# Performance work log

Hardware: AMD Instinct MI355X
Metric: run time of the kernel (lower is better)

## Reference

```python
import jax, jax.numpy as jnp
import numpy as np

E, H = 1024, 16
B, N = 4, 2048
D = E // H

def setup_inputs() -> dict:
    key = jax.random.key(0)
    ks = jax.random.split(key, 5)
    s = 1.0 / np.sqrt(E)
    return {
        "x": jax.random.normal(ks[0], (B, N, E), dtype=jnp.float32),
        "Wqkv": jax.random.normal(ks[1], (E, 3 * E), dtype=jnp.float32) * s,
        "bqkv": jnp.zeros((3 * E,), dtype=jnp.float32),
        "Wproj": jax.random.normal(ks[2], (E, E), dtype=jnp.float32) * s,
        "bproj": jnp.zeros((E,), dtype=jnp.float32),
    }

def reference(x, Wqkv, bqkv, Wproj, bproj):
    b, n, e = x.shape
    qkv = x @ Wqkv + bqkv  # [b, n, 3e]
    # torch rearrange 'b n (h d qkv) -> qkv b h n d': last dim splits as (h, d, 3)
    qkv = qkv.reshape(b, n, H, D, 3)
    qkv = jnp.transpose(qkv, (4, 0, 2, 1, 3))  # [3, b, h, n, d]
    q, k, v = qkv[0], qkv[1], qkv[2]
    # NOTE: module scales by 1/sqrt(e) (full embed dim), faithfully reproduced
    att = jax.nn.softmax(jnp.einsum('bhqd,bhkd->bhqk', q, k) / jnp.sqrt(jnp.float32(E)), axis=-1)
    out = jnp.einsum('bhqk,bhkd->bhqd', att, v)  # dropout is identity in eval
    out = jnp.transpose(out, (0, 2, 1, 3)).reshape(b, n, e)  # 'b h n d -> b n (h d)'
    return out @ Wproj + bproj
```

## Files before the change

### kernel.cpp

```cpp
#include <hip/hip_runtime.h>
#include <stdint.h>

typedef unsigned short u16;
typedef __attribute__((ext_vector_type(8))) short short8;
typedef __attribute__((ext_vector_type(4))) float f32x4;

#define LOG2E 1.44269504088896340736f
#define CS (0.03125f * LOG2E)
#define BB 4
#define NN 2048
#define EE 1024
#define HH 16
#define DD 64
#define MM 8192
#define C3 3072

#if __has_builtin(__builtin_amdgcn_exp2f)
#define EXP2(x) __builtin_amdgcn_exp2f(x)
#else
#define EXP2(x) exp2f(x)
#endif

__device__ __forceinline__ u16 f2bf(float f) {
  union { float f; unsigned u; } v; v.f = f;
  unsigned r = v.u + 0x7fffu + ((v.u >> 16) & 1u);
  return (u16)(r >> 16);
}

#if __has_builtin(__builtin_amdgcn_cvt_pk_bf16_f32)
typedef __attribute__((ext_vector_type(2))) __bf16 bf16x2;
__device__ __forceinline__ unsigned pk2(float a, float b) {
  union { bf16x2 v; unsigned u; } c;
  c.v = __builtin_amdgcn_cvt_pk_bf16_f32(a, b);
  return c.u;
}
#else
__device__ __forceinline__ unsigned pk2(float a, float b) {
  union { float f; unsigned u; } x, y; x.f = a; y.f = b;
  return ((x.u + 0x8000u) >> 16) | ((y.u + 0x8000u) & 0xffff0000u);
}
#endif

__device__ __forceinline__ void async16(const void* g, void* l) {
  __builtin_amdgcn_global_load_lds((const __attribute__((address_space(1))) void*)g,
                                   (__attribute__((address_space(3))) void*)l,
                                   16, 0, 0);
}

__device__ __forceinline__ int vperm(int t) {
  return (t & 0x23) | ((t & 8) << 1) | ((t & 4) << 1) | ((t & 16) >> 2);
}

__global__ __launch_bounds__(256) void prep_kernel(const float* __restrict__ x, u16* __restrict__ xb,
                                                   const float* __restrict__ Wqkv, u16* __restrict__ WqkvT,
                                                   const float* __restrict__ Wproj, u16* __restrict__ WprojT) {
  __shared__ float tile[32][33];
  const int bid = blockIdx.x;
  if (bid < 8192) {
    int i = (bid * 256 + threadIdx.x) * 4;
    float4 v = *(const float4*)(x + i);
    ushort4 o; o.x = f2bf(v.x); o.y = f2bf(v.y); o.z = f2bf(v.z); o.w = f2bf(v.w);
    *(ushort4*)(xb + i) = o;
    return;
  }
  const int permute = bid < 11264 ? 1 : 0;
  const float* W = permute ? Wqkv : Wproj;
  u16* Wt = permute ? WqkvT : WprojT;
  const int ncols = permute ? C3 : EE;
  const int t = permute ? bid - 8192 : bid - 11264;
  const int nbx = permute ? 96 : 32;
  const int c0 = (t % nbx) * 32, k0 = (t / nbx) * 32;
  const int tx = threadIdx.x & 31, ty = threadIdx.x >> 5;
#pragma unroll
  for (int r = 0; r < 32; r += 8)
    tile[ty + r][tx] = W[(size_t)(k0 + ty + r) * ncols + c0 + tx];
  __syncthreads();
#pragma unroll
  for (int r = 0; r < 32; r += 8) {
    int c = c0 + ty + r;
    int cp = c;
    if (permute) {
      int tt = c % 3, hh = c / 192, d = (c / 3) % 64;
      cp = tt * 1024 + hh * 64 + d;
    }
    Wt[(size_t)cp * EE + k0 + tx] = f2bf(tile[tx][ty + r]);
  }
}

template <int KDIM, int MI>
__device__ __forceinline__ void gemm_core(const u16* __restrict__ A, const u16* __restrict__ Bt,
                                          int m0, int n0, u16* As, u16* Bs, f32x4 (*acc)[4]) {
  constexpr int L2M = (MI == 8) ? 3 : 2;
  constexpr int ACH = MI * 128;
  constexpr int ALD = MI / 2;
  constexpr int ASZ = ACH * 8;
  constexpr int NT = KDIM / 32;
  const int tid = threadIdx.x, lane = tid & 63, wave = tid >> 6;
  const int wm = wave >> 1, wn = wave & 1;

#pragma unroll
  for (int i = 0; i < MI; i++)
#pragma unroll
    for (int j = 0; j < 4; j++) acc[i][j] = (f32x4){0.f, 0.f, 0.f, 0.f};

  auto stage = [&](int t, int slot) {
    const u16* Ab = A + (size_t)m0 * KDIM + t * 32;
    const u16* Bb = Bt + (size_t)n0 * KDIM + t * 32;
#pragma unroll
    for (int i = 0; i < ALD; i++) {
      int c = i * 256 + tid;
      int r = c & 15, qc = (c >> 4) & 3, mi = (c >> 6) & (MI - 1), wmc = c >> (6 + L2M);
      int row = (wmc * MI + mi) * 16 + r;
      async16(Ab + (size_t)row * KDIM + qc * 8, &As[slot * ASZ + c * 8]);
    }
#pragma unroll
    for (int i = 0; i < 2; i++) {
      int c = i * 256 + tid;
      int r = c & 15, qc = (c >> 4) & 3, ci = (c >> 6) & 3, wnc = c >> 8;
      int row = (wnc * 4 + ci) * 16 + r;
      async16(Bb + (size_t)row * KDIM + qc * 8, &Bs[slot * 4096 + c * 8]);
    }
  };

  stage(0, 0);
  stage(1, 1);
  if constexpr (MI == 8) asm volatile("s_waitcnt vmcnt(6)" ::: "memory");
  else                   asm volatile("s_waitcnt vmcnt(4)" ::: "memory");
  __builtin_amdgcn_s_barrier();

  for (int t = 0; t < NT; ++t) {
    const int slot = t % 3;
    if (t + 2 < NT) stage(t + 2, (t + 2) % 3);
    short8 af[MI], bf[4];
    const u16* Ar = As + slot * ASZ + (wm * (MI * 64) + lane) * 8;
#pragma unroll
    for (int mi = 0; mi < MI; mi++) af[mi] = *(const short8*)(Ar + mi * 512);
    const u16* Br = Bs + slot * 4096 + (wn * 256 + lane) * 8;
#pragma unroll
    for (int ci = 0; ci < 4; ci++) bf[ci] = *(const short8*)(Br + ci * 512);
    __builtin_amdgcn_s_setprio(1);
#pragma unroll
    for (int mi = 0; mi < MI; mi++)
#pragma unroll
      for (int ci = 0; ci < 4; ci++)
        acc[mi][ci] = __builtin_amdgcn_mfma_f32_16x16x32_bf16(af[mi], bf[ci], acc[mi][ci], 0, 0, 0);
    __builtin_amdgcn_s_setprio(0);
    if (t + 2 < NT) {
      if constexpr (MI == 8) asm volatile("s_waitcnt vmcnt(6)" ::: "memory");
      else                   asm volatile("s_waitcnt vmcnt(4)" ::: "memory");
      __builtin_amdgcn_s_barrier();
    } else if (t + 1 < NT) {
      asm volatile("s_waitcnt vmcnt(0)" ::: "memory");
      __builtin_amdgcn_s_barrier();
    }
  }
}


__global__ __launch_bounds__(256, 2) void gemm_qkv(const u16* __restrict__ Xb, const u16* __restrict__ Wt,
                                                   const float* __restrict__ bqkv, u16* __restrict__ Qb,
                                                   u16* __restrict__ KVt) {
  __shared__ __align__(16) u16 As[3 * 8192];
  __shared__ __align__(16) u16 Bs[3 * 4096];
  f32x4 acc[8][4];
  const int m0 = blockIdx.y * 256, n0 = blockIdx.x * 128;
  gemm_core<EE, 8>(Xb, Wt, m0, n0, As, Bs, acc);
  const int tid = threadIdx.x, lane = tid & 63, wave = tid >> 6;
  const int q = lane >> 4, r16 = lane & 15;
  const int wm = wave >> 1, wn = wave & 1;
  const int wrow = wm * 128, wcol = wn * 64;
  const int t = n0 >> 10;
  const int b = m0 >> 11;
#pragma unroll
  for (int ci = 0; ci < 4; ci++) {
    const int cp = n0 + wcol + ci * 16 + r16;
    const int hh = (cp >> 6) & 15, d = cp & 63;
    const float bias = bqkv[hh * 192 + d * 3 + t];
    if (t == 0) {
#pragma unroll
      for (int mi = 0; mi < 8; mi++)
#pragma unroll
        for (int r = 0; r < 4; r++) {
          const int m = m0 + wrow + mi * 16 + q * 4 + r;
          Qb[((size_t)(b * 16 + hh) * 2048 + (m & 2047)) * 64 + d] = f2bf((acc[mi][ci][r] + bias) * CS);
        }
    } else if (t == 1) {
      const size_t bhbase = (size_t)(b * 16 + hh) * 32;
      const size_t dpart = (size_t)(d >> 5) * 2048 + ((d >> 3) & 3) * 128 + (d & 7);
#pragma unroll
      for (int mi = 0; mi < 8; mi++)
#pragma unroll
        for (int r = 0; r < 4; r++) {
          const int key = (m0 + wrow + mi * 16 + q * 4 + r) & 2047;
          KVt[(bhbase + (key >> 6)) * 8192 + dpart + ((key >> 4) & 3) * 512 + (key & 15) * 8] =
              f2bf(acc[mi][ci][r] + bias);
        }
    } else {
      const size_t bhbase = (size_t)(b * 16 + hh) * 32;
      const int dpart = (d >> 4) * 512 + (d & 15) * 8;
#pragma unroll
      for (int mi = 0; mi < 8; mi++) {
        const int nb = (m0 + wrow + mi * 16 + q * 4) & 2047;
        const int sb = vperm(nb & 63);
        ushort4 w;
        w.x = f2bf(acc[mi][ci][0] + bias);
        w.y = f2bf(acc[mi][ci][1] + bias);
        w.z = f2bf(acc[mi][ci][2] + bias);
        w.w = f2bf(acc[mi][ci][3] + bias);
        *(ushort4*)&KVt[(bhbase + (nb >> 6)) * 8192 + 4096 + (sb >> 5) * 2048 +
                        ((sb >> 3) & 3) * 128 + dpart + (sb & 7)] = w;
      }
    }
  }
}

__global__ __launch_bounds__(256, 3) void gemm_proj(const u16* __restrict__ Ob, const u16* __restrict__ Wt,
                                                    const float* __restrict__ bp, float* __restrict__ out) {
  __shared__ __align__(16) u16 As[3 * 4096];
  __shared__ __align__(16) u16 Bs[3 * 4096];
  f32x4 acc[4][4];
  const int m0 = blockIdx.y * 128, n0 = blockIdx.x * 128;
  gemm_core<EE, 4>(Ob, Wt, m0, n0, As, Bs, acc);
  const int tid = threadIdx.x, lane = tid & 63, wave = tid >> 6;
  const int q = lane >> 4, r16 = lane & 15;
  const int wrow = (wave >> 1) * 64, wcol = (wave & 1) * 64;
#pragma unroll
  for (int ci = 0; ci < 4; ci++) {
    const int col = n0 + wcol + ci * 16 + r16;
    const float bias = bp[col];
#pragma unroll
    for (int mi = 0; mi < 4; mi++)
#pragma unroll
      for (int r = 0; r < 4; r++) {
        const int m = m0 + wrow + mi * 16 + q * 4 + r;
        out[(size_t)m * EE + col] = acc[mi][ci][r] + bias;
      }
  }
}

__global__ __launch_bounds__(256, 4) void attn_kernel(const u16* __restrict__ Qg, const u16* __restrict__ KVg,
                                                      u16* __restrict__ Ob) {
  __shared__ __align__(16) u16 KVd[2][8192];
  const int tid = threadIdx.x, lane = tid & 63, wave = tid >> 6;
  const int q = lane >> 4, r16 = lane & 15;
  const int id = blockIdx.x + 16 * blockIdx.y;
  const int g = id & 7, s = id >> 3;
  const int bh = g * 8 + (s >> 4);
  const int q0 = (s & 15) * 128;
  const u16* Qp = Qg + ((size_t)bh * NN + q0) * DD;
  const u16* KVp = KVg + (size_t)bh * (32 * 8192);

  short8 qf[2][2];
#pragma unroll
  for (int nj = 0; nj < 2; nj++)
#pragma unroll
    for (int ks = 0; ks < 2; ks++)
      qf[nj][ks] = *(const short8*)(Qp + (wave * 32 + nj * 16 + r16) * 64 + ks * 32 + q * 8);

#pragma unroll
  for (int i = 0; i < 4; i++) {
    int c = i * 256 + tid;
    async16(KVp + c * 8, &KVd[0][c * 8]);
  }
  __syncthreads();

  f32x4 o[2][4];
  f32x4 ol[2];
#pragma unroll
  for (int i = 0; i < 2; i++) {
    ol[i] = (f32x4){0.f, 0.f, 0.f, 0.f};
#pragma unroll
    for (int j = 0; j < 4; j++) o[i][j] = (f32x4){0.f, 0.f, 0.f, 0.f};
  }
  const short8 ones = {16256, 16256, 16256, 16256, 16256, 16256, 16256, 16256};

  for (int j = 0; j < 32; j++) {
    const int buf = j & 1;
    if (j < 31) {
      const u16* src = KVp + (size_t)(j + 1) * 8192;
#pragma unroll
      for (int i = 0; i < 4; i++) {
        int c = i * 256 + tid;
        async16(src + c * 8, &KVd[buf ^ 1][c * 8]);
      }
    }

    f32x4 st[4][2];
#pragma unroll
    for (int mi = 0; mi < 4; mi++)
#pragma unroll
      for (int nj = 0; nj < 2; nj++) st[mi][nj] = (f32x4){0.f, 0.f, 0.f, 0.f};
#pragma unroll
    for (int ks = 0; ks < 2; ks++) {
      short8 kf[4];
#pragma unroll
      for (int mi = 0; mi < 4; mi++)
        kf[mi] = *(const short8*)&KVd[buf][ks * 2048 + mi * 512 + lane * 8];
#pragma unroll
      for (int mi = 0; mi < 4; mi++)
#pragma unroll
        for (int nj = 0; nj < 2; nj++)
          st[mi][nj] = __builtin_amdgcn_mfma_f32_16x16x32_bf16(kf[mi], qf[nj][ks], st[mi][nj], 0, 0, 0);
    }

    uint2 pka[4][2];
#pragma unroll
    for (int mi = 0; mi < 4; mi++)
#pragma unroll
      for (int nj = 0; nj < 2; nj++) {
        float p0 = EXP2(st[mi][nj][0]);
        float p1 = EXP2(st[mi][nj][1]);
        float p2 = EXP2(st[mi][nj][2]);
        float p3 = EXP2(st[mi][nj][3]);
        pka[mi][nj].x = pk2(p0, p1);
        pka[mi][nj].y = pk2(p2, p3);
      }

#pragma unroll
    for (int kp = 0; kp < 2; kp++) {
      short8 vf[4];
#pragma unroll
      for (int ci = 0; ci < 4; ci++)
        vf[ci] = *(const short8*)&KVd[buf][4096 + kp * 2048 + ci * 512 + lane * 8];
#pragma unroll
      for (int ri = 0; ri < 2; ri++) {
        union { uint4 u; short8 s; } a;
        a.u.x = pka[2 * kp][ri].x;
        a.u.y = pka[2 * kp][ri].y;
        a.u.z = pka[2 * kp + 1][ri].x;
        a.u.w = pka[2 * kp + 1][ri].y;
#pragma unroll
        for (int ci = 0; ci < 4; ci++)
          o[ri][ci] = __builtin_amdgcn_mfma_f32_16x16x32_bf16(a.s, vf[ci], o[ri][ci], 0, 0, 0);
        ol[ri] = __builtin_amdgcn_mfma_f32_16x16x32_bf16(a.s, ones, ol[ri], 0, 0, 0);
      }
    }

    __syncthreads();
  }

  const int b = bh >> 4, h = bh & 15;
#pragma unroll
  for (int ri = 0; ri < 2; ri++)
#pragma unroll
    for (int r = 0; r < 4; r++) {
      const float inv = 1.0f / ol[ri][r];
      const int n = q0 + wave * 32 + ri * 16 + q * 4 + r;
#pragma unroll
      for (int ci = 0; ci < 4; ci++) {
        const int d = ci * 16 + r16;
        Ob[((size_t)(b * NN + n)) * EE + h * 64 + d] = f2bf(o[ri][ci][r] * inv);
      }
    }
}


extern "C" void kernel_launch(void* const* d_in, const int* in_sizes, int n_in,
                              void* d_out, int out_size, void* d_ws, size_t ws_size,
                              hipStream_t stream) {
  const float* x     = (const float*)d_in[0];
  const float* Wqkv  = (const float*)d_in[1];
  const float* bqkv  = (const float*)d_in[2];
  const float* Wproj = (const float*)d_in[3];
  const float* bproj = (const float*)d_in[4];
  float* out = (float*)d_out;
  char* ws = (char*)d_ws;

  u16* Xb     = (u16*)(ws);
  u16* Ob     = Xb;
  u16* Qb     = (u16*)(ws + (size_t)(16 << 20));
  u16* KVt    = (u16*)(ws + (size_t)(32 << 20));
  u16* WqkvT  = (u16*)(ws + (size_t)(64 << 20));
  u16* WprojT = (u16*)(ws + (size_t)(72 << 20));

  prep_kernel<<<12288, 256, 0, stream>>>(x, Xb, Wqkv, WqkvT, Wproj, WprojT);
  gemm_qkv<<<dim3(24, 32), 256, 0, stream>>>(Xb, WqkvT, bqkv, Qb, KVt);
  attn_kernel<<<dim3(16, 64), 256, 0, stream>>>(Qb, KVt, Ob);
  gemm_proj<<<dim3(8, 64), 256, 0, stream>>>(Ob, WprojT, bproj, out);
}
```

Measured before the change: 299.2 us.

## Rework both GEMMs into 256x256 8-wave tiles with interleaved quarter-step prefetch

```diff
diff --git a/kernel.cpp b/kernel.cpp
--- a/kernel.cpp
+++ b/kernel.cpp
@@ -87,93 +87,157 @@
   }
 }
 
-template <int KDIM, int MI>
-__device__ __forceinline__ void gemm_core(const u16* __restrict__ A, const u16* __restrict__ Bt,
-                                          int m0, int n0, u16* As, u16* Bs, f32x4 (*acc)[4]) {
-  constexpr int L2M = (MI == 8) ? 3 : 2;
-  constexpr int ACH = MI * 128;
-  constexpr int ALD = MI / 2;
-  constexpr int ASZ = ACH * 8;
-  constexpr int NT = KDIM / 32;
+template <int KDIM>
+__device__ __forceinline__ void gemm_core8(const u16* __restrict__ A, const u16* __restrict__ Bt,
+                                           int m0, int n0, u16* As, u16* Bs, f32x4 (*acc)[4]) {
+  constexpr int NT = KDIM / 64;
   const int tid = threadIdx.x, lane = tid & 63, wave = tid >> 6;
-  const int wm = wave >> 1, wn = wave & 1;
-
-#pragma unroll
-  for (int i = 0; i < MI; i++)
+  const int wm = wave >> 2, wn = wave & 3;
+
+#pragma unroll
+  for (int i = 0; i < 8; i++)
 #pragma unroll
     for (int j = 0; j < 4; j++) acc[i][j] = (f32x4){0.f, 0.f, 0.f, 0.f};
 
-  auto stage = [&](int t, int slot) {
-    const u16* Ab = A + (size_t)m0 * KDIM + t * 32;
-    const u16* Bb = Bt + (size_t)n0 * KDIM + t * 32;
-#pragma unroll
-    for (int i = 0; i < ALD; i++) {
-      int c = i * 256 + tid;
-      int r = c & 15, qc = (c >> 4) & 3, mi = (c >> 6) & (MI - 1), wmc = c >> (6 + L2M);
-      int row = (wmc * MI + mi) * 16 + r;
-      async16(Ab + (size_t)row * KDIM + qc * 8, &As[slot * ASZ + c * 8]);
-    }
+  auto stageA = [&](int t, int h) {
+    const u16* Ab = A + (size_t)m0 * KDIM + t * 64;
+    u16* dst = As + (t & 1) * 16384;
 #pragma unroll
     for (int i = 0; i < 2; i++) {
-      int c = i * 256 + tid;
-      int r = c & 15, qc = (c >> 4) & 3, ci = (c >> 6) & 3, wnc = c >> 8;
-      int row = (wnc * 4 + ci) * 16 + r;
-      async16(Bb + (size_t)row * KDIM + qc * 8, &Bs[slot * 4096 + c * 8]);
+      int j = i * 512 + tid;
+      int lj = j & 63, mi_l = (j >> 6) & 3, wmj = (j >> 8) & 1, ksj = (j >> 9) & 1;
+      int mi = h * 4 + mi_l;
+      int c = ((ksj * 2 + wmj) * 8 + mi) * 64 + lj;
+      int row = wmj * 128 + mi * 16 + (lj & 15);
+      int k = ksj * 32 + (lj >> 4) * 8;
+      async16(Ab + (size_t)row * KDIM + k, dst + c * 8);
     }
   };
-
-  stage(0, 0);
-  stage(1, 1);
-  if constexpr (MI == 8) asm volatile("s_waitcnt vmcnt(6)" ::: "memory");
-  else                   asm volatile("s_waitcnt vmcnt(4)" ::: "memory");
+  auto stageB = [&](int t, int cset) {
+    const u16* Bb = Bt + (size_t)n0 * KDIM + t * 64;
+    u16* dst = Bs + (t & 1) * 16384;
+#pragma unroll
+    for (int i = 0; i < 2; i++) {
+      int j = i * 512 + tid;
+      int lj = j & 63, ci_l = (j >> 6) & 1, wnj = (j >> 7) & 3, ksj = (j >> 9) & 1;
+      int ci = cset * 2 + ci_l;
+      int c = ((ksj * 4 + wnj) * 4 + ci) * 64 + lj;
+      int row = wnj * 64 + ci * 16 + (lj & 15);
+      int k = ksj * 32 + (lj >> 4) * 8;
+      async16(Bb + (size_t)row * KDIM + k, dst + c * 8);
+    }
+  };
+
+  stageA(0, 0); stageB(0, 0); stageB(0, 1); stageA(0, 1);
+  asm volatile("s_waitcnt vmcnt(4)" ::: "memory");
   __builtin_amdgcn_s_barrier();
 
+  short8 af[4][2], bf[4][2];
+#pragma unroll 2
   for (int t = 0; t < NT; ++t) {
-    const int slot = t % 3;
-    if (t + 2 < NT) stage(t + 2, (t + 2) % 3);
-    short8 af[MI], bf[4];
-    const u16* Ar = As + slot * ASZ + (wm * (MI * 64) + lane) * 8;
-#pragma unroll
-    for (int mi = 0; mi < MI; mi++) af[mi] = *(const short8*)(Ar + mi * 512);
-    const u16* Br = Bs + slot * 4096 + (wn * 256 + lane) * 8;
-#pragma unroll
-    for (int ci = 0; ci < 4; ci++) bf[ci] = *(const short8*)(Br + ci * 512);
+    const int buf = t & 1;
+    const u16* Ab = As + buf * 16384;
+    const u16* Bb = Bs + buf * 16384;
+    const bool pf = (t + 1 < NT);
+
+#pragma unroll
+    for (int m = 0; m < 4; m++)
+#pragma unroll
+      for (int ks = 0; ks < 2; ks++)
+        af[m][ks] = *(const short8*)&Ab[(((ks * 2 + wm) * 8 + m) * 64 + lane) * 8];
+#pragma unroll
+    for (int c = 0; c < 2; c++)
+#pragma unroll
+      for (int ks = 0; ks < 2; ks++)
+        bf[c][ks] = *(const short8*)&Bb[(((ks * 4 + wn) * 4 + c) * 64 + lane) * 8];
+    if (pf) stageA(t + 1, 0);
+    __builtin_amdgcn_s_barrier();
     __builtin_amdgcn_s_setprio(1);
 #pragma unroll
-    for (int mi = 0; mi < MI; mi++)
-#pragma unroll
-      for (int ci = 0; ci < 4; ci++)
-        acc[mi][ci] = __builtin_amdgcn_mfma_f32_16x16x32_bf16(af[mi], bf[ci], acc[mi][ci], 0, 0, 0);
+    for (int m = 0; m < 4; m++)
+#pragma unroll
+      for (int c = 0; c < 2; c++)
+#pragma unroll
+        for (int ks = 0; ks < 2; ks++)
+          acc[m][c] = __builtin_amdgcn_mfma_f32_16x16x32_bf16(af[m][ks], bf[c][ks], acc[m][c], 0, 0, 0);
     __builtin_amdgcn_s_setprio(0);
-    if (t + 2 < NT) {
-      if constexpr (MI == 8) asm volatile("s_waitcnt vmcnt(6)" ::: "memory");
-      else                   asm volatile("s_waitcnt vmcnt(4)" ::: "memory");
+    if (pf) asm volatile("s_waitcnt vmcnt(4)" ::: "memory");
+    else    asm volatile("s_waitcnt vmcnt(2)" ::: "memory");
+    __builtin_amdgcn_s_barrier();
+
+#pragma unroll
+    for (int c = 2; c < 4; c++)
+#pragma unroll
+      for (int ks = 0; ks < 2; ks++)
+        bf[c][ks] = *(const short8*)&Bb[(((ks * 4 + wn) * 4 + c) * 64 + lane) * 8];
+    if (pf) stageB(t + 1, 0);
+    __builtin_amdgcn_s_barrier();
+    __builtin_amdgcn_s_setprio(1);
+#pragma unroll
+    for (int m = 0; m < 4; m++)
+#pragma unroll
+      for (int c = 2; c < 4; c++)
+#pragma unroll
+        for (int ks = 0; ks < 2; ks++)
+          acc[m][c] = __builtin_amdgcn_mfma_f32_16x16x32_bf16(af[m][ks], bf[c][ks], acc[m][c], 0, 0, 0);
+    __builtin_amdgcn_s_setprio(0);
+    if (pf) asm volatile("s_waitcnt vmcnt(4)" ::: "memory");
+    else    asm volatile("s_waitcnt vmcnt(0)" ::: "memory");
+    __builtin_amdgcn_s_barrier();
+
+#pragma unroll
+    for (int m = 0; m < 4; m++)
+#pragma unroll
+      for (int ks = 0; ks < 2; ks++)
+        af[m][ks] = *(const short8*)&Ab[(((ks * 2 + wm) * 8 + 4 + m) * 64 + lane) * 8];
+    if (pf) stageB(t + 1, 1);
+    __builtin_amdgcn_s_barrier();
+    __builtin_amdgcn_s_setprio(1);
+#pragma unroll
+    for (int m = 0; m < 4; m++)
+#pragma unroll
+      for (int c = 0; c < 2; c++)
+#pragma unroll
+        for (int ks = 0; ks < 2; ks++)
+          acc[4 + m][c] = __builtin_amdgcn_mfma_f32_16x16x32_bf16(af[m][ks], bf[c][ks], acc[4 + m][c], 0, 0, 0);
+    __builtin_amdgcn_s_setprio(0);
+    __builtin_amdgcn_s_barrier();
+
+    if (pf) stageA(t + 1, 1);
+    __builtin_amdgcn_s_barrier();
+    __builtin_amdgcn_s_setprio(1);
+#pragma unroll
+    for (int m = 0; m < 4; m++)
+#pragma unroll
+      for (int c = 2; c < 4; c++)
+#pragma unroll
+        for (int ks = 0; ks < 2; ks++)
+          acc[4 + m][c] = __builtin_amdgcn_mfma_f32_16x16x32_bf16(af[m][ks], bf[c][ks], acc[4 + m][c], 0, 0, 0);
+    __builtin_amdgcn_s_setprio(0);
+    if (pf) {
+      asm volatile("s_waitcnt vmcnt(4)" ::: "memory");
       __builtin_amdgcn_s_barrier();
-    } else if (t + 1 < NT) {
-      asm volatile("s_waitcnt vmcnt(0)" ::: "memory");
-      __builtin_amdgcn_s_barrier();
-    }
-  }
-}
-
-
-__global__ __launch_bounds__(256, 2) void gemm_qkv(const u16* __restrict__ Xb, const u16* __restrict__ Wt,
+    }
+  }
+}
+
+
+__global__ __launch_bounds__(512, 1) void gemm_qkv(const u16* __restrict__ Xb, const u16* __restrict__ Wt,
                                                    const float* __restrict__ bqkv, u16* __restrict__ Qb,
                                                    u16* __restrict__ KVt) {
-  __shared__ __align__(16) u16 As[3 * 8192];
-  __shared__ __align__(16) u16 Bs[3 * 4096];
+  __shared__ __align__(16) u16 As[2 * 16384];
+  __shared__ __align__(16) u16 Bs[2 * 16384];
   f32x4 acc[8][4];
-  const int m0 = blockIdx.y * 256, n0 = blockIdx.x * 128;
-  gemm_core<EE, 8>(Xb, Wt, m0, n0, As, Bs, acc);
+  const int m0 = blockIdx.y * 256, n0 = blockIdx.x * 256;
+  gemm_core8<EE>(Xb, Wt, m0, n0, As, Bs, acc);
   const int tid = threadIdx.x, lane = tid & 63, wave = tid >> 6;
   const int q = lane >> 4, r16 = lane & 15;
-  const int wm = wave >> 1, wn = wave & 1;
-  const int wrow = wm * 128, wcol = wn * 64;
+  const int wm = wave >> 2, wn = wave & 3;
   const int t = n0 >> 10;
   const int b = m0 >> 11;
 #pragma unroll
   for (int ci = 0; ci < 4; ci++) {
-    const int cp = n0 + wcol + ci * 16 + r16;
+    const int cp = n0 + wn * 64 + ci * 16 + r16;
     const int hh = (cp >> 6) & 15, d = cp & 63;
     const float bias = bqkv[hh * 192 + d * 3 + t];
     if (t == 0) {
@@ -181,7 +245,7 @@
       for (int mi = 0; mi < 8; mi++)
 #pragma unroll
         for (int r = 0; r < 4; r++) {
-          const int m = m0 + wrow + mi * 16 + q * 4 + r;
+          const int m = m0 + wm * 128 + mi * 16 + q * 4 + r;
           Qb[((size_t)(b * 16 + hh) * 2048 + (m & 2047)) * 64 + d] = f2bf((acc[mi][ci][r] + bias) * CS);
         }
     } else if (t == 1) {
@@ -191,7 +255,7 @@
       for (int mi = 0; mi < 8; mi++)
 #pragma unroll
         for (int r = 0; r < 4; r++) {
-          const int key = (m0 + wrow + mi * 16 + q * 4 + r) & 2047;
+          const int key = (m0 + wm * 128 + mi * 16 + q * 4 + r) & 2047;
           KVt[(bhbase + (key >> 6)) * 8192 + dpart + ((key >> 4) & 3) * 512 + (key & 15) * 8] =
               f2bf(acc[mi][ci][r] + bias);
         }
@@ -200,7 +264,7 @@
       const int dpart = (d >> 4) * 512 + (d & 15) * 8;
 #pragma unroll
       for (int mi = 0; mi < 8; mi++) {
-        const int nb = (m0 + wrow + mi * 16 + q * 4) & 2047;
+        const int nb = (m0 + wm * 128 + mi * 16 + q * 4) & 2047;
         const int sb = vperm(nb & 63);
         ushort4 w;
         w.x = f2bf(acc[mi][ci][0] + bias);
@@ -214,25 +278,25 @@
   }
 }
 
-__global__ __launch_bounds__(256, 3) void gemm_proj(const u16* __restrict__ Ob, const u16* __restrict__ Wt,
+__global__ __launch_bounds__(512, 1) void gemm_proj(const u16* __restrict__ Ob, const u16* __restrict__ Wt,
                                                     const float* __restrict__ bp, float* __restrict__ out) {
-  __shared__ __align__(16) u16 As[3 * 4096];
-  __shared__ __align__(16) u16 Bs[3 * 4096];
-  f32x4 acc[4][4];
-  const int m0 = blockIdx.y * 128, n0 = blockIdx.x * 128;
-  gemm_core<EE, 4>(Ob, Wt, m0, n0, As, Bs, acc);
+  __shared__ __align__(16) u16 As[2 * 16384];
+  __shared__ __align__(16) u16 Bs[2 * 16384];
+  f32x4 acc[8][4];
+  const int m0 = blockIdx.y * 256, n0 = blockIdx.x * 256;
+  gemm_core8<EE>(Ob, Wt, m0, n0, As, Bs, acc);
   const int tid = threadIdx.x, lane = tid & 63, wave = tid >> 6;
   const int q = lane >> 4, r16 = lane & 15;
-  const int wrow = (wave >> 1) * 64, wcol = (wave & 1) * 64;
+  const int wm = wave >> 2, wn = wave & 3;
 #pragma unroll
   for (int ci = 0; ci < 4; ci++) {
-    const int col = n0 + wcol + ci * 16 + r16;
+    const int col = n0 + wn * 64 + ci * 16 + r16;
     const float bias = bp[col];
 #pragma unroll
-    for (int mi = 0; mi < 4; mi++)
+    for (int mi = 0; mi < 8; mi++)
 #pragma unroll
       for (int r = 0; r < 4; r++) {
-        const int m = m0 + wrow + mi * 16 + q * 4 + r;
+        const int m = m0 + wm * 128 + mi * 16 + q * 4 + r;
         out[(size_t)m * EE + col] = acc[mi][ci][r] + bias;
       }
   }
@@ -374,7 +438,7 @@
   u16* WprojT = (u16*)(ws + (size_t)(72 << 20));
 
   prep_kernel<<<12288, 256, 0, stream>>>(x, Xb, Wqkv, WqkvT, Wproj, WprojT);
-  gemm_qkv<<<dim3(24, 32), 256, 0, stream>>>(Xb, WqkvT, bqkv, Qb, KVt);
+  gemm_qkv<<<dim3(12, 32), 512, 0, stream>>>(Xb, WqkvT, bqkv, Qb, KVt);
   attn_kernel<<<dim3(16, 64), 256, 0, stream>>>(Qb, KVt, Ob);
-  gemm_proj<<<dim3(8, 64), 256, 0, stream>>>(Ob, WprojT, bproj, out);
-}
+  gemm_proj<<<dim3(4, 32), 512, 0, stream>>>(Ob, WprojT, bproj, out);
+}
```

Result: slower. 315.1 us (+5.3%).
